# Kernel tuning notes

Measured on AMD Instinct MI355X. Metric: run time of the kernel, lower is better.

The kernel has to match this reference:

```python
import jax, jax.numpy as jnp
import numpy as np

B, S, D = 2, 2048, 512   # batch, seq_len, input_dim
H, E = 8, 512            # num_heads, per-head output_dim (full D per head, per source)
NEG = -1e9


def setup_inputs() -> dict:
    key = jax.random.key(0)
    ks = jax.random.split(key, 12)
    sc = 1.0 / np.sqrt(D)
    inp = {
        "query": jax.random.normal(ks[0], (B, S, D), jnp.float32),
        "key":   jax.random.normal(ks[1], (B, S, D), jnp.float32),
        "value": jax.random.normal(ks[2], (B, S, D), jnp.float32),
        "mask":  jax.random.randint(ks[3], (B, S, S), 0, 2).astype(bool),
        # stacked per-head Linear weights: [H, D, E] (x @ W layout)
        "Wq": jax.random.normal(ks[4], (H, D, E), jnp.float32) * sc,
        "bq": jax.random.normal(ks[5], (H, E), jnp.float32) * 0.02,
        "Wk": jax.random.normal(ks[6], (H, D, E), jnp.float32) * sc,
        "bk": jax.random.normal(ks[7], (H, E), jnp.float32) * 0.02,
        "Wv": jax.random.normal(ks[8], (H, D, E), jnp.float32) * sc,
        "bv": jax.random.normal(ks[9], (H, E), jnp.float32) * 0.02,
        # output projection: Linear(H*E, E)
        "Wo": jax.random.normal(ks[10], (H * E, E), jnp.float32) * (1.0 / np.sqrt(H * E)),
        "bo": jax.random.normal(ks[11], (E,), jnp.float32) * 0.02,
    }
    return inp


def reference(query, key, value, mask, Wq, bq, Wk, bk, Wv, bv, Wo, bo):
    # Batched per-head projections (replaces the Python per-head loop)
    q = jnp.einsum("bsd,hde->bhse", query, Wq) + bq[None, :, None, :]
    k = jnp.einsum("bsd,hde->bhse", key,   Wk) + bk[None, :, None, :]
    v = jnp.einsum("bsd,hde->bhse", value, Wv) + bv[None, :, None, :]
    # NOTE: source has NO 1/sqrt(d) scaling — kept faithful.
    scores = jnp.einsum("bhse,bhte->bhst", q, k)           # [B,H,S,S]
    scores = jnp.where(mask[:, None, :, :], scores, NEG)    # masked_fill(mask==0, -1e9)
    attn = jax.nn.softmax(scores, axis=-1)
    out = jnp.einsum("bhst,bhte->bhse", attn, v)            # [B,H,S,E]
    # concat heads along last dim in head order -> [B,S,H*E]
    cat = out.transpose(0, 2, 1, 3).reshape(out.shape[0], out.shape[2], -1)
    return cat @ Wo + bo
```

## Files before the change

kernel.cpp:

```cpp
#include <hip/hip_runtime.h>

#define B_  2
#define S_  2048
#define D_  512
#define H_  8
#define E_  512
#define HE_ 4096

typedef _Float16 half8_t  __attribute__((ext_vector_type(8)));
typedef _Float16 half4_t  __attribute__((ext_vector_type(4)));
typedef float    floatx4  __attribute__((ext_vector_type(4)));
typedef __attribute__((address_space(1))) const unsigned int* gas_ptr;
typedef __attribute__((address_space(3))) unsigned int*       las_ptr;

__global__ __launch_bounds__(256) void cast3_f16_kernel(
    const float* __restrict__ s0, const float* __restrict__ s1, const float* __restrict__ s2,
    _Float16* __restrict__ d0, _Float16* __restrict__ d1, _Float16* __restrict__ d2, int n4) {
    int i = blockIdx.x * 256 + threadIdx.x;
    if (i >= n4) return;
    const float* s = (blockIdx.y == 0) ? s0 : (blockIdx.y == 1) ? s1 : s2;
    _Float16*    d = (blockIdx.y == 0) ? d0 : (blockIdx.y == 1) ? d1 : d2;
    float4 v = ((const float4*)s)[i];
    half4_t h = { (_Float16)v.x, (_Float16)v.y, (_Float16)v.z, (_Float16)v.w };
    ((half4_t*)d)[i] = h;
}

__global__ __launch_bounds__(256) void transpose3_cast_kernel(
    const float* __restrict__ p0, const float* __restrict__ p1, const float* __restrict__ p2,
    _Float16* __restrict__ q0, _Float16* __restrict__ q1, _Float16* __restrict__ q2,
    int R, int C) {
    __shared__ float t[32][33];
    int which = blockIdx.z >> 3, hh = blockIdx.z & 7;
    const float* src = ((which == 0) ? p0 : (which == 1) ? p1 : p2) + (long long)hh * R * C;
    _Float16*    dst = ((which == 0) ? q0 : (which == 1) ? q1 : q2) + (long long)hh * R * C;
    int c0 = blockIdx.x * 32, r0 = blockIdx.y * 32;
    int tx = threadIdx.x, ty = threadIdx.y;
#pragma unroll
    for (int i = 0; i < 32; i += 8)
        t[ty + i][tx] = src[(long long)(r0 + ty + i) * C + (c0 + tx)];
    __syncthreads();
#pragma unroll
    for (int i = 0; i < 32; i += 8)
        dst[(long long)(c0 + ty + i) * R + (r0 + tx)] = (_Float16)t[tx][ty + i];
}

__global__ __launch_bounds__(256) void transpose_cast_kernel(const float* __restrict__ src,
                                                             _Float16* __restrict__ dst,
                                                             int R, int C) {
    __shared__ float t[32][33];
    int c0 = blockIdx.x * 32, r0 = blockIdx.y * 32;
    int tx = threadIdx.x, ty = threadIdx.y;
#pragma unroll
    for (int i = 0; i < 32; i += 8)
        t[ty + i][tx] = src[(long long)(r0 + ty + i) * C + (c0 + tx)];
    __syncthreads();
#pragma unroll
    for (int i = 0; i < 32; i += 8)
        dst[(long long)(c0 + ty + i) * R + (r0 + tx)] = (_Float16)t[tx][ty + i];
}

__device__ __forceinline__ void xcd_decode(int& z, int& by, int& bx) {
    int gx = gridDim.x, gy = gridDim.y, gz = gridDim.z;
    int bpz = gx * gy;
    int fid = blockIdx.x + gx * (blockIdx.y + gy * blockIdx.z);
    if ((gz & 7) == 0) {
        int xcd = fid & 7, sl = fid >> 3;
        int zg = gz >> 3;
        z = xcd * zg + sl / bpz;
        int inner = sl % bpz;
        by = inner / gx;
        bx = inner % gx;
    } else {
        z = blockIdx.z; by = blockIdx.y; bx = blockIdx.x;
    }
}

__device__ __forceinline__ void bt256_core(
    const _Float16* __restrict__ A, const _Float16* __restrict__ Bt,
    int lda, int ldb, int nt, int m0, int n0,
    _Float16 (*As)[256][32], _Float16 (*Bs)[256][32],
    floatx4 (&acc)[8][4])
{
    int tid  = threadIdx.x;
    int wave = tid >> 6, lane = tid & 63;
    int quad = lane >> 4, l16 = lane & 15;
    int wm128 = (wave >> 2) * 128;
    int wn64  = (wave & 3) * 64;
    int wave16 = wave * 16;
    int sr = lane >> 2;
    int scg = ((lane & 3) ^ ((lane >> 3) & 3)) * 8;
    int cra = (quad ^ ((l16 >> 1) & 3)) * 8;

    const _Float16* gA0 = A + (long long)(m0 + wave16 + sr) * lda + scg;
    const _Float16* gB0 = Bt + (long long)(n0 + wave16 + sr) * ldb + scg;

    auto STAGE = [&](int t) {
        int buf = t & 3;
        const _Float16* gA = gA0 + (t << 5);
        const _Float16* gB = gB0 + (t << 5);
        _Float16* lA = &As[buf][wave16][0];
        _Float16* lB = &Bs[buf][wave16][0];
#pragma unroll
        for (int j = 0; j < 2; j++) {
            __builtin_amdgcn_global_load_lds((gas_ptr)(gA + (long long)(j * 128) * lda),
                                             (las_ptr)(lA + j * 128 * 32), 16, 0, 0);
            __builtin_amdgcn_global_load_lds((gas_ptr)(gB + (long long)(j * 128) * ldb),
                                             (las_ptr)(lB + j * 128 * 32), 16, 0, 0);
        }
    };
    auto DSREAD = [&](int t, half8_t (&fa)[8], half8_t (&fb)[4]) {
        int buf = t & 3;
#pragma unroll
        for (int i = 0; i < 8; i++)
            fa[i] = *(const half8_t*)&As[buf][wm128 + i * 16 + l16][cra];
#pragma unroll
        for (int i = 0; i < 4; i++)
            fb[i] = *(const half8_t*)&Bs[buf][wn64 + i * 16 + l16][cra];
    };
    auto MFMA = [&](half8_t (&fa)[8], half8_t (&fb)[4]) {
        __builtin_amdgcn_s_setprio(1);
#pragma unroll
        for (int mi = 0; mi < 8; mi++)
#pragma unroll
            for (int ni = 0; ni < 4; ni++)
                acc[mi][ni] = __builtin_amdgcn_mfma_f32_16x16x32_f16(fa[mi], fb[ni], acc[mi][ni], 0, 0, 0);
        __builtin_amdgcn_s_setprio(0);
    };
    auto BODY = [&](int t, half8_t (&ca)[8], half8_t (&cb)[4],
                    half8_t (&na)[8], half8_t (&nb)[4]) {
        if (t + 3 < nt) {
            STAGE(t + 3);
            asm volatile("s_waitcnt vmcnt(8)" ::: "memory");
            __builtin_amdgcn_s_barrier();
        } else if (t + 3 == nt) {
            asm volatile("s_waitcnt vmcnt(4)" ::: "memory");
            __builtin_amdgcn_s_barrier();
        } else if (t + 2 == nt) {
            asm volatile("s_waitcnt vmcnt(0)" ::: "memory");
            __builtin_amdgcn_s_barrier();
        }
        if (t + 1 < nt) DSREAD(t + 1, na, nb);
        MFMA(ca, cb);
        asm volatile("s_waitcnt lgkmcnt(0)" ::: "memory");
        __builtin_amdgcn_sched_barrier(0);
    };

    half8_t fa0[8], fb0[4], fa1[8], fb1[4];

    STAGE(0); STAGE(1); STAGE(2);
    asm volatile("s_waitcnt vmcnt(8)" ::: "memory");
    __builtin_amdgcn_s_barrier();
    DSREAD(0, fa0, fb0);
    asm volatile("s_waitcnt lgkmcnt(0)" ::: "memory");
    __builtin_amdgcn_sched_barrier(0);

    for (int t0 = 0; t0 < nt; t0 += 2) {
        BODY(t0,     fa0, fb0, fa1, fb1);
        BODY(t0 + 1, fa1, fb1, fa0, fb0);
    }
}

__global__ __launch_bounds__(512, 2) void gemm_bt256_kernel(
    const _Float16* __restrict__ A, const _Float16* __restrict__ Bt,
    _Float16* __restrict__ C,
    int K, int lda, int ldb,
    long long a_z, long long b_z, long long c_b, long long c_h, int c_rs, int hdiv)
{
    int z, byy, bxx;
    xcd_decode(z, byy, bxx);
    int bb = z / hdiv, hh = z % hdiv;
    A  += (long long)z * a_z;
    Bt += (long long)z * b_z;
    _Float16* Cz = C + bb * c_b + hh * c_h;

    int m0 = byy * 256;
    int n0 = bxx * 256;

    __shared__ __align__(16) _Float16 As[4][256][32];
    __shared__ __align__(16) _Float16 Bs[4][256][32];

    floatx4 acc[8][4] = {};
    bt256_core(A, Bt, lda, ldb, K >> 5, m0, n0, As, Bs, acc);

    int tid  = threadIdx.x;
    int wave = tid >> 6, lane = tid & 63;
    int quad = lane >> 4, l16 = lane & 15;
    int wm128 = (wave >> 2) * 128;
    int wn64  = (wave & 3) * 64;
#pragma unroll
    for (int mi = 0; mi < 8; mi++)
#pragma unroll
        for (int ni = 0; ni < 4; ni++)
#pragma unroll
            for (int r = 0; r < 4; r++) {
                int row = m0 + wm128 + mi * 16 + quad * 4 + r;
                int col = n0 + wn64 + ni * 16 + l16;
                Cz[(long long)row * c_rs + col] = (_Float16)acc[mi][ni][r];
            }
}

__global__ __launch_bounds__(512, 2) void gemm_qkv256_kernel(
    const _Float16* __restrict__ Xq, const _Float16* __restrict__ Xk, const _Float16* __restrict__ Xv,
    const _Float16* __restrict__ WqT, const _Float16* __restrict__ WkT, const _Float16* __restrict__ WvT,
    const float* __restrict__ bq, const float* __restrict__ bk, const float* __restrict__ bv,
    _Float16* __restrict__ Qb, _Float16* __restrict__ Kb, _Float16* __restrict__ VT)
{
    int z, byy, bxx;
    xcd_decode(z, byy, bxx);
    int which = z >> 4, zz = z & 15;
    int bb = zz >> 3, hh = zz & 7;
    const _Float16* A  = ((which == 0) ? Xq : (which == 1) ? Xk : Xv) + (long long)bb * S_ * D_;
    const _Float16* Bt = ((which == 0) ? WqT : (which == 1) ? WkT : WvT) + (long long)hh * E_ * D_;
    const float* bias  = ((which == 0) ? bq : (which == 1) ? bk : bv) + hh * E_;

    int m0 = byy * 256;
    int n0 = bxx * 256;

    __shared__ __align__(16) _Float16 As[4][256][32];
    __shared__ __align__(16) _Float16 Bs[4][256][32];

    floatx4 acc[8][4] = {};
    bt256_core(A, Bt, D_, D_, D_ / 32, m0, n0, As, Bs, acc);

    int tid  = threadIdx.x;
    int wave = tid >> 6, lane = tid & 63;
    int quad = lane >> 4, l16 = lane & 15;
    int wm128 = (wave >> 2) * 128;
    int wn64  = (wave & 3) * 64;

    if (which < 2) {
        _Float16* C = ((which == 0) ? Qb : Kb) + ((long long)(bb * H_ + hh)) * S_ * E_;
#pragma unroll
        for (int mi = 0; mi < 8; mi++)
#pragma unroll
            for (int ni = 0; ni < 4; ni++)
#pragma unroll
                for (int r = 0; r < 4; r++) {
                    int row = m0 + wm128 + mi * 16 + quad * 4 + r;
                    int col = n0 + wn64 + ni * 16 + l16;
                    C[(long long)row * E_ + col] = (_Float16)(acc[mi][ni][r] + bias[col]);
                }
    } else {
        _Float16* C = VT + ((long long)(bb * H_ + hh)) * E_ * S_;
#pragma unroll
        for (int mi = 0; mi < 8; mi++)
#pragma unroll
            for (int ni = 0; ni < 4; ni++) {
                int row = m0 + wm128 + mi * 16 + quad * 4;
                int col = n0 + wn64 + ni * 16 + l16;
                float bcol = bias[col];
                half4_t h4 = { (_Float16)(acc[mi][ni][0] + bcol), (_Float16)(acc[mi][ni][1] + bcol),
                               (_Float16)(acc[mi][ni][2] + bcol), (_Float16)(acc[mi][ni][3] + bcol) };
                *(half4_t*)(C + (long long)col * S_ + row) = h4;
            }
    }
}

__global__ __launch_bounds__(512) void softmax_mask8_kernel(_Float16* __restrict__ sc,
                                                            const int* __restrict__ mask)
{
    int b = blockIdx.z, s = blockIdx.x;
    int wave = threadIdx.x >> 6, lane = threadIdx.x & 63;
    _Float16* row = sc + ((long long)(b * H_ + wave) * S_ + s) * S_;
    const int* mrow = mask + ((long long)b * S_ + s) * S_;

    half8_t h[4];
    float v[32];
    float mx = -3.0e38f;
#pragma unroll
    for (int j = 0; j < 4; j++) {
        int c = j * 512 + lane * 8;
        h[j] = *(const half8_t*)(row + c);
        int4 mA = *(const int4*)(mrow + c);
        int4 mB = *(const int4*)(mrow + c + 4);
        int mm[8] = { mA.x, mA.y, mA.z, mA.w, mB.x, mB.y, mB.z, mB.w };
#pragma unroll
        for (int e = 0; e < 8; e++) {
            float val = mm[e] ? (float)h[j][e] : -1.0e9f;
            v[j * 8 + e] = val;
            mx = fmaxf(mx, val);
        }
    }
#pragma unroll
    for (int o = 32; o > 0; o >>= 1) mx = fmaxf(mx, __shfl_xor(mx, o));

    float sum = 0.0f;
#pragma unroll
    for (int i = 0; i < 32; i++) { v[i] = __expf(v[i] - mx); sum += v[i]; }
#pragma unroll
    for (int o = 32; o > 0; o >>= 1) sum += __shfl_xor(sum, o);

    float inv = 1.0f / sum;
#pragma unroll
    for (int j = 0; j < 4; j++) {
#pragma unroll
        for (int e = 0; e < 8; e++) h[j][e] = (_Float16)(v[j * 8 + e] * inv);
        *(half8_t*)(row + j * 512 + lane * 8) = h[j];
    }
}

__global__ __launch_bounds__(256) void gemm_bt_n64_splitk_kernel(
    const _Float16* __restrict__ A, const _Float16* __restrict__ Bt,
    const float* __restrict__ bias, float* __restrict__ C,
    int K, int lda, int ldb, int ldc, int ksplit)
{
    int m0 = blockIdx.y * 128;
    int n0 = blockIdx.x * 64;
    int kchunk = K / ksplit;
    int kbeg = blockIdx.z * kchunk;
    int kend = kbeg + kchunk;

    __shared__ __align__(16) _Float16 As[128][32];
    __shared__ __align__(16) _Float16 Bs[64][32];

    int tid  = threadIdx.x;
    int wave = tid >> 6, lane = tid & 63;
    int quad = lane >> 4, l16 = lane & 15;
    int wy = (wave >> 1) * 64, wx = (wave & 1) * 32;

    int srow = (wave << 4) + (lane >> 2);
    int scg = ((lane & 3) ^ ((lane >> 3) & 3)) * 8;
    _Float16* lA0 = &As[0][0] + (wave << 9);
    _Float16* lB0 = &Bs[0][0] + (wave << 9);
    int cra = (quad ^ ((l16 >> 1) & 3)) * 8;

    floatx4 acc[4][2] = {};

    for (int k0 = kbeg; k0 < kend; k0 += 32) {
        if (k0 != kbeg) __syncthreads();
        const _Float16* gA = A + (long long)(m0 + srow) * lda + k0 + scg;
        const _Float16* gB = Bt + (long long)(n0 + srow) * ldb + k0 + scg;
#pragma unroll
        for (int j = 0; j < 2; j++)
            __builtin_amdgcn_global_load_lds((gas_ptr)(gA + (long long)(j << 6) * lda),
                                             (las_ptr)(lA0 + (j << 11)), 16, 0, 0);
        __builtin_amdgcn_global_load_lds((gas_ptr)gB, (las_ptr)lB0, 16, 0, 0);
        __syncthreads();

        half8_t af[4], bf[2];
#pragma unroll
        for (int i = 0; i < 4; i++)
            af[i] = *(const half8_t*)&As[wy + i * 16 + l16][cra];
#pragma unroll
        for (int i = 0; i < 2; i++)
            bf[i] = *(const half8_t*)&Bs[wx + i * 16 + l16][cra];
#pragma unroll
        for (int mi = 0; mi < 4; mi++)
#pragma unroll
            for (int ni = 0; ni < 2; ni++)
                acc[mi][ni] = __builtin_amdgcn_mfma_f32_16x16x32_f16(af[mi], bf[ni], acc[mi][ni], 0, 0, 0);
    }

    int addb = (blockIdx.z == 0) && bias;
#pragma unroll
    for (int mi = 0; mi < 4; mi++)
#pragma unroll
        for (int ni = 0; ni < 2; ni++)
#pragma unroll
            for (int r = 0; r < 4; r++) {
                int row = m0 + wy + mi * 16 + quad * 4 + r;
                int col = n0 + wx + ni * 16 + l16;
                float v = acc[mi][ni][r];
                if (addb) v += bias[col];
                atomicAdd(&C[(long long)row * ldc + col], v);
            }
}

extern "C" void kernel_launch(void* const* d_in, const int* in_sizes, int n_in,
                              void* d_out, int out_size, void* d_ws, size_t ws_size,
                              hipStream_t stream)
{
    const float* qin = (const float*)d_in[0];
    const float* kin = (const float*)d_in[1];
    const float* vin = (const float*)d_in[2];
    const int*   mask = (const int*)d_in[3];
    const float* Wq = (const float*)d_in[4];
    const float* bq = (const float*)d_in[5];
    const float* Wk = (const float*)d_in[6];
    const float* bk = (const float*)d_in[7];
    const float* Wv = (const float*)d_in[8];
    const float* bv = (const float*)d_in[9];
    const float* Wo = (const float*)d_in[10];
    const float* bo = (const float*)d_in[11];
    float* out = (float*)d_out;

    char* ws = (char*)d_ws;
    size_t off = 0;
    _Float16* WoT = (_Float16*)(ws + off); off += (size_t)E_ * HE_ * 2;
    _Float16* Qb  = (_Float16*)(ws + off); off += (size_t)B_ * H_ * S_ * E_ * 2;
    _Float16* Kb  = (_Float16*)(ws + off); off += (size_t)B_ * H_ * S_ * E_ * 2;
    _Float16* VT  = (_Float16*)(ws + off); off += (size_t)B_ * H_ * E_ * S_ * 2;
    size_t region = off;
    _Float16* Xq  = (_Float16*)(ws + region);
    _Float16* Xk  = Xq  + (size_t)B_ * S_ * D_;
    _Float16* Xv  = Xk  + (size_t)B_ * S_ * D_;
    _Float16* WqT = Xv  + (size_t)B_ * S_ * D_;
    _Float16* WkT = WqT + (size_t)H_ * E_ * D_;
    _Float16* WvT = WkT + (size_t)H_ * E_ * D_;
    _Float16* SC  = (_Float16*)(ws + region);
    _Float16* cat = Qb;

    long long SE = (long long)S_ * E_;
    long long SS = (long long)S_ * S_;
    long long ES = (long long)E_ * S_;

    (void)hipMemsetAsync(d_out, 0, (size_t)out_size * sizeof(float), stream);

    int n4 = B_ * S_ * D_ / 4;
    cast3_f16_kernel<<<dim3(n4 / 256, 3), 256, 0, stream>>>(qin, kin, vin, Xq, Xk, Xv, n4);

    dim3 tb(32, 8);
    transpose3_cast_kernel<<<dim3(E_ / 32, D_ / 32, 24), tb, 0, stream>>>(
        Wq, Wk, Wv, WqT, WkT, WvT, D_, E_);
    transpose_cast_kernel<<<dim3(E_ / 32, HE_ / 32, 1), tb, 0, stream>>>(Wo, WoT, HE_, E_);

    gemm_qkv256_kernel<<<dim3(E_ / 256, S_ / 256, 48), 512, 0, stream>>>(
        Xq, Xk, Xv, WqT, WkT, WvT, bq, bk, bv, Qb, Kb, VT);

    gemm_bt256_kernel<<<dim3(S_ / 256, S_ / 256, B_ * H_), 512, 0, stream>>>(
        Qb, Kb, SC, E_, E_, E_, SE, SE, 0, SS, S_, 32 );

    softmax_mask8_kernel<<<dim3(S_, 1, B_), 512, 0, stream>>>(SC, mask);

    gemm_bt256_kernel<<<dim3(E_ / 256, S_ / 256, B_ * H_), 512, 0, stream>>>(
        SC, VT, cat, S_, S_, S_, SS, ES, (long long)S_ * HE_, E_, HE_, H_);

    gemm_bt_n64_splitk_kernel<<<dim3(E_ / 64, (B_ * S_) / 128, 4), 256, 0, stream>>>(
        cat, WoT, bo, out, HE_, HE_, HE_, E_, 4);
}
```

Before: 519.0 us.

## Split GEMM mainloop into two half-tile phases interleaving A/B staging

Restructures the 256x256 GEMM main loop from a register double-buffered scheme (prefetch whole next k-tile fragments) into two half phases per k-step. Each phase reads half of the A fragments, issues one operand's async global-to-LDS load, and runs 16 MFMAs. This roughly halves the fragment registers, which may ease register pressure at 2 blocks per CU. In exchange it adds more barriers per iteration and loses the overlap of the LDS reads with the previous MFMAs.

```diff
diff --git a/kernel.cpp b/kernel.cpp
--- a/kernel.cpp
+++ b/kernel.cpp
@@ -94,69 +94,77 @@
     const _Float16* gA0 = A + (long long)(m0 + wave16 + sr) * lda + scg;
     const _Float16* gB0 = Bt + (long long)(n0 + wave16 + sr) * ldb + scg;
 
-    auto STAGE = [&](int t) {
+    auto STAGE_A = [&](int t) {
         int buf = t & 3;
         const _Float16* gA = gA0 + (t << 5);
-        const _Float16* gB = gB0 + (t << 5);
         _Float16* lA = &As[buf][wave16][0];
-        _Float16* lB = &Bs[buf][wave16][0];
-#pragma unroll
-        for (int j = 0; j < 2; j++) {
+#pragma unroll
+        for (int j = 0; j < 2; j++)
             __builtin_amdgcn_global_load_lds((gas_ptr)(gA + (long long)(j * 128) * lda),
                                              (las_ptr)(lA + j * 128 * 32), 16, 0, 0);
+    };
+    auto STAGE_B = [&](int t) {
+        int buf = t & 3;
+        const _Float16* gB = gB0 + (t << 5);
+        _Float16* lB = &Bs[buf][wave16][0];
+#pragma unroll
+        for (int j = 0; j < 2; j++)
             __builtin_amdgcn_global_load_lds((gas_ptr)(gB + (long long)(j * 128) * ldb),
                                              (las_ptr)(lB + j * 128 * 32), 16, 0, 0);
-        }
     };
-    auto DSREAD = [&](int t, half8_t (&fa)[8], half8_t (&fb)[4]) {
+    auto RD_A = [&](int t, int h, half8_t (&fa)[4]) {
         int buf = t & 3;
 #pragma unroll
-        for (int i = 0; i < 8; i++)
-            fa[i] = *(const half8_t*)&As[buf][wm128 + i * 16 + l16][cra];
+        for (int i = 0; i < 4; i++)
+            fa[i] = *(const half8_t*)&As[buf][wm128 + (h * 4 + i) * 16 + l16][cra];
+    };
+    auto RD_B = [&](int t, half8_t (&fb)[4]) {
+        int buf = t & 3;
 #pragma unroll
         for (int i = 0; i < 4; i++)
             fb[i] = *(const half8_t*)&Bs[buf][wn64 + i * 16 + l16][cra];
     };
-    auto MFMA = [&](half8_t (&fa)[8], half8_t (&fb)[4]) {
+    auto MFMA16 = [&](int h, half8_t (&fa)[4], half8_t (&fb)[4]) {
         __builtin_amdgcn_s_setprio(1);
 #pragma unroll
-        for (int mi = 0; mi < 8; mi++)
+        for (int mi = 0; mi < 4; mi++)
 #pragma unroll
             for (int ni = 0; ni < 4; ni++)
-                acc[mi][ni] = __builtin_amdgcn_mfma_f32_16x16x32_f16(fa[mi], fb[ni], acc[mi][ni], 0, 0, 0);
+                acc[h * 4 + mi][ni] =
+                    __builtin_amdgcn_mfma_f32_16x16x32_f16(fa[mi], fb[ni], acc[h * 4 + mi][ni], 0, 0, 0);
         __builtin_amdgcn_s_setprio(0);
     };
-    auto BODY = [&](int t, half8_t (&ca)[8], half8_t (&cb)[4],
-                    half8_t (&na)[8], half8_t (&nb)[4]) {
-        if (t + 3 < nt) {
-            STAGE(t + 3);
-            asm volatile("s_waitcnt vmcnt(8)" ::: "memory");
-            __builtin_amdgcn_s_barrier();
-        } else if (t + 3 == nt) {
-            asm volatile("s_waitcnt vmcnt(4)" ::: "memory");
-            __builtin_amdgcn_s_barrier();
-        } else if (t + 2 == nt) {
-            asm volatile("s_waitcnt vmcnt(0)" ::: "memory");
-            __builtin_amdgcn_s_barrier();
-        }
-        if (t + 1 < nt) DSREAD(t + 1, na, nb);
-        MFMA(ca, cb);
+
+    STAGE_A(0); STAGE_B(0); STAGE_A(1); STAGE_B(1); STAGE_A(2); STAGE_B(2);
+    asm volatile("s_waitcnt vmcnt(8)" ::: "memory");
+    __builtin_amdgcn_s_barrier();
+
+    half8_t faL[4], faH[4], fb[4];
+
+    for (int t = 0; t < nt; ++t) {
+        RD_A(t, 0, faL);
+        RD_B(t, fb);
+        if (t + 3 < nt) STAGE_A(t + 3);
+        __builtin_amdgcn_sched_barrier(0);
+        __builtin_amdgcn_s_barrier();
         asm volatile("s_waitcnt lgkmcnt(0)" ::: "memory");
         __builtin_amdgcn_sched_barrier(0);
-    };
-
-    half8_t fa0[8], fb0[4], fa1[8], fb1[4];
-
-    STAGE(0); STAGE(1); STAGE(2);
-    asm volatile("s_waitcnt vmcnt(8)" ::: "memory");
-    __builtin_amdgcn_s_barrier();
-    DSREAD(0, fa0, fb0);
-    asm volatile("s_waitcnt lgkmcnt(0)" ::: "memory");
-    __builtin_amdgcn_sched_barrier(0);
-
-    for (int t0 = 0; t0 < nt; t0 += 2) {
-        BODY(t0,     fa0, fb0, fa1, fb1);
-        BODY(t0 + 1, fa1, fb1, fa0, fb0);
+        MFMA16(0, faL, fb);
+        __builtin_amdgcn_s_barrier();
+
+        RD_A(t, 1, faH);
+        if (t + 3 < nt) STAGE_B(t + 3);
+        if (t + 1 < nt) {
+            if (t + 3 < nt)       asm volatile("s_waitcnt vmcnt(8)" ::: "memory");
+            else if (t + 3 == nt) asm volatile("s_waitcnt vmcnt(4)" ::: "memory");
+            else                  asm volatile("s_waitcnt vmcnt(0)" ::: "memory");
+        }
+        __builtin_amdgcn_sched_barrier(0);
+        __builtin_amdgcn_s_barrier();
+        asm volatile("s_waitcnt lgkmcnt(0)" ::: "memory");
+        __builtin_amdgcn_sched_barrier(0);
+        MFMA16(1, faH, fb);
+        __builtin_amdgcn_s_barrier();
     }
 }
 
```

Result: faster. 487.8 us (-6.0%).
